# Performance work log

Hardware: AMD Instinct MI355X
Metric: run time of the kernel (lower is better)

Reference implementation:

```python
import jax, jax.numpy as jnp
import numpy as np
from jax import lax

GRID_SIZE = 3


def setup_inputs() -> dict:
    key = jax.random.key(0)
    k1, k2, k3 = jax.random.split(key, 3)
    B, Cin, Cout, H, W, KH, KW, G = 32, 64, 64, 64, 64, 3, 3, GRID_SIZE
    x = jax.random.normal(k1, (B, Cin, H, W), dtype=jnp.float32)
    scale_base = jax.random.normal(k2, (Cout, Cin, KH, KW), dtype=jnp.float32) * 0.1
    scale_spline = jnp.ones((Cout, Cin, KH, KW), dtype=jnp.float32)
    coeff = jax.random.normal(k3, (2, Cout, Cin, KH, KW, G), dtype=jnp.float32) * 0.02
    bias = jnp.zeros((Cout,), dtype=jnp.float32)
    return {"x": x, "scale_base": scale_base, "scale_spline": scale_spline, "coeff": coeff, "bias": bias}


def _conv(x, w, padding=1):
    return lax.conv_general_dilated(
        x, w, window_strides=(1, 1), padding=((padding, padding), (padding, padding)),
        dimension_numbers=("NCHW", "OIHW", "NCHW"))


def reference(x, scale_base, scale_spline, coeff, bias):
    B, Cin, H, W = x.shape
    Cout, _, KH, KW = scale_base.shape
    G = coeff.shape[-1]
    # Fourier feature expansion: cos(k*x), sin(k*x) for k = 1..G
    ks = jnp.arange(1, G + 1, dtype=x.dtype)
    xk = x[:, :, None] * ks[None, None, :, None, None]          # (B, Cin, G, H, W)
    feats = jnp.concatenate([jnp.cos(xk), jnp.sin(xk)], axis=2)  # (B, Cin, 2G, H, W)
    feats = feats.reshape(B, Cin * 2 * G, H, W)
    # Spline weights: coeff (2, Cout, Cin, KH, KW, G) scaled per-tap -> (Cout, Cin*2G, KH, KW)
    w = coeff * scale_spline[None, :, :, :, :, None]
    w = jnp.transpose(w, (1, 2, 0, 5, 3, 4)).reshape(Cout, Cin * 2 * G, KH, KW)
    # Base branch: SiLU(x) convolved with scale_base
    base = jax.nn.silu(x)
    out = _conv(base, scale_base) + _conv(feats, w)
    out = out + bias[None, :, None, None]
    return out
```

## Files before the change

### kernel.cpp

```cpp
#include <hip/hip_runtime.h>

typedef __attribute__((ext_vector_type(8))) short bf16x8;
typedef __attribute__((ext_vector_type(4))) float f32x4;

#define FROW   4224
#define FBUF   42240
#define BGRP   36864
#define LDS_TOT (2 * FBUF + 2 * BGRP)

static __device__ __forceinline__ unsigned short f2bf(float f) {
  union { float f; unsigned u; } v; v.f = f;
  unsigned r = v.u + 0x7fffu + ((v.u >> 16) & 1u);
  return (unsigned short)(r >> 16);
}

static __device__ __forceinline__ void gload16(const void* g, void* l) {
  __builtin_amdgcn_global_load_lds(
      (const __attribute__((address_space(1))) void*)g,
      (__attribute__((address_space(3))) void*)l, 16, 0, 0);
}

__global__ void pack_w_k(const float* __restrict__ sb, const float* __restrict__ ss,
                         const float* __restrict__ cf, unsigned short* __restrict__ wpk) {
  int idx = blockIdx.x * 256 + threadIdx.x;
  if (idx >= 126 * 64 * 32) return;
  int e = idx & 7;
  int q = (idx >> 3) & 3;
  int co = (idx >> 5) & 63;
  int rest = idx >> 11;
  int tap = rest % 9;
  int c2 = rest / 9;
  int c = c2 >> 1, half = c2 & 1;
  int ci = half * 32 + q * 8 + e;
  int kh = tap / 3, kw = tap % 3;
  int wi = ((co * 64 + ci) * 3 + kh) * 3 + kw;
  float v;
  if (c == 0) {
    v = sb[wi];
  } else {
    int s = (c - 1) / 3, g = (c - 1) % 3;
    v = cf[(s * 36864 + wi) * 3 + g] * ss[wi];
  }
  wpk[((c2 * 9 + tap) * 64 + co) * 32 + ((q ^ ((co >> 1) & 3)) << 3) + e] = f2bf(v);
}

__global__ void feats_k(const float* __restrict__ x, unsigned short* __restrict__ fg) {
  __shared__ __align__(16) unsigned short lds[64 * 456];
  const int b = blockIdx.x, h = blockIdx.y;
  const int tid = threadIdx.x;
  const int w = tid & 63, cig = tid >> 6;
  const int key = ((w + 1) >> 1) & 3;
  const int base = w * 456;
#pragma unroll
  for (int i = 0; i < 16; ++i) {
    int ci = cig * 16 + i;
    float v = x[(((size_t)b * 64 + ci) * 64 + h) * 64 + w];
    float sg = 1.0f / (1.0f + __expf(-v));
    float f0 = v * sg;
    float s1, c1;
    __sincosf(v, &s1, &c1);
    float c2v = c1 * c1 - s1 * s1, s2v = 2.0f * s1 * c1;
    float c3v = c1 * c2v - s1 * s2v, s3v = s1 * c2v + c1 * s2v;
    int q = ci >> 3;
    int half = q >> 2, qq = q & 3;
    int sl = (half * 4 + (qq ^ key)) * 8 + (ci & 7);
    lds[base + 0 * 64 + sl] = f2bf(f0);
    lds[base + 1 * 64 + sl] = f2bf(c1);
    lds[base + 2 * 64 + sl] = f2bf(c2v);
    lds[base + 3 * 64 + sl] = f2bf(c3v);
    lds[base + 4 * 64 + sl] = f2bf(s1);
    lds[base + 5 * 64 + sl] = f2bf(s2v);
    lds[base + 6 * 64 + sl] = f2bf(s3v);
  }
  __syncthreads();
#pragma unroll
  for (int k = 0; k < 14; ++k) {
    int u = tid + k * 256;
    int qs = u & 3;
    int ww = (u >> 2) & 63;
    int c2i = u >> 8;
    int cc = c2i >> 1, half = c2i & 1;
    uint4 v = *(const uint4*)&lds[ww * 456 + cc * 64 + (half * 4 + qs) * 8];
    unsigned short* dst = fg + ((size_t)(c2i * 32 + b) * 64 + h) * 2048 + (ww * 4 + qs) * 8;
    *(uint4*)dst = v;
  }
}

__global__ __launch_bounds__(512, 2) void gemm_k(
    const unsigned short* __restrict__ fg, const unsigned short* __restrict__ wpk,
    const float* __restrict__ bias, float* __restrict__ out) {
  extern __shared__ __align__(16) char smem[];
  const int b = blockIdx.x;
  const int h0 = blockIdx.y * 8;
  const int tid = threadIdx.x;
  const int lane = tid & 63;
  const int wid = tid >> 6;
  const int l15 = lane & 15;
  const int lg = lane >> 4;
  const int grp = wid >> 2;
  const int rowb = (wid & 3) * 2;
  const char* fgB = (const char*)fg;
  const char* wpkB = (const char*)wpk;

  for (int i = tid; i < 2 * FBUF / 4; i += 512) {
    int off = i * 4;
    int off2 = (off >= FBUF) ? off - FBUF : off;
    int row = off2 / FROW;
    int cb = off2 - row * FROW;
    int hh = h0 - 1 + row;
    bool staged = ((unsigned)hh < 64u) && (cb >= 64) && (cb < 4160);
    if (!staged) ((int*)smem)[i] = 0;
  }

  int aoff[4][3], boff[4];
#pragma unroll
  for (int cf = 0; cf < 4; ++cf) {
#pragma unroll
    for (int kw = 0; kw < 3; ++kw) {
      int col = cf * 16 + l15 + kw;
      aoff[cf][kw] = col * 64 + ((lg ^ ((col >> 1) & 3)) << 4);
    }
    int co = cf * 16 + l15;
    boff[cf] = co * 64 + ((lg ^ ((co >> 1) & 3)) << 4);
  }

#define STAGE_GRP(cn, fdst, bdst)                                                \
  for (int u = wid; u < 76; u += 8) {                                            \
    if (u < 40) {                                                                \
      int row = u >> 2, j = u & 3;                                               \
      int hh = h0 - 1 + row;                                                     \
      if ((unsigned)hh < 64u)                                                    \
        gload16(fgB + ((size_t)((cn) * 2048 + b * 64 + hh)) * 4096 +             \
                    j * 1024 + lane * 16,                                        \
                (fdst) + row * FROW + 64 + j * 1024);                            \
    } else {                                                                     \
      int t = u - 40;                                                            \
      int tap = t >> 2, part = t & 3;                                            \
      gload16(wpkB + (size_t)((cn) * 9 + tap) * 4096 + part * 1024 + lane * 16,  \
              (bdst) + tap * 4096 + part * 1024);                                \
    }                                                                            \
  }

  STAGE_GRP(0, smem, smem + 2 * FBUF);
  __syncthreads();

  f32x4 acc[2][4][4];
#pragma unroll
  for (int ro = 0; ro < 2; ++ro)
#pragma unroll
    for (int cfi = 0; cfi < 4; ++cfi)
#pragma unroll
      for (int nf = 0; nf < 4; ++nf)
#pragma unroll
        for (int qq = 0; qq < 4; ++qq) acc[ro][cfi][nf][qq] = 0.0f;

#define LOADT(T, Ar, Br)                                                         \
  {                                                                              \
    const int kh_ = (T) / 3, kw_ = (T) % 3;                                      \
    const char* r0 = f + (rowb + kh_) * FROW;                                    \
    const char* r1 = r0 + FROW;                                                  \
    _Pragma("unroll")                                                            \
    for (int cfi = 0; cfi < 4; ++cfi) {                                          \
      Ar[0][cfi] = *(const bf16x8*)(r0 + aoff[cfi][kw_]);                        \
      Ar[1][cfi] = *(const bf16x8*)(r1 + aoff[cfi][kw_]);                        \
    }                                                                            \
    _Pragma("unroll")                                                            \
    for (int nf = 0; nf < 4; ++nf)                                               \
      Br[nf] = *(const bf16x8*)(bgc + (T) * 4096 + boff[nf]);                    \
  }
#define MFMAT(Ar, Br)                                                            \
  {                                                                              \
    _Pragma("unroll")                                                            \
    for (int ro = 0; ro < 2; ++ro)                                               \
      _Pragma("unroll")                                                          \
      for (int cfi = 0; cfi < 4; ++cfi)                                          \
        _Pragma("unroll")                                                        \
        for (int nf = 0; nf < 4; ++nf)                                           \
          acc[ro][cfi][nf] = __builtin_amdgcn_mfma_f32_16x16x32_bf16(            \
              Ar[ro][cfi], Br[nf], acc[ro][cfi][nf], 0, 0, 0);                   \
  }

#define SGB(m, n) __builtin_amdgcn_sched_group_barrier((m), (n), 0);

  for (int c2 = 0; c2 < 14; ++c2) {
    const int cur = c2 & 1;
    const char* f = smem + (cur ? FBUF : 0);
    const char* bgc = smem + 2 * FBUF + (cur ? BGRP : 0);
    if (c2 < 13) {
      char* fnext = smem + (cur ? 0 : FBUF);
      char* bnext = smem + 2 * FBUF + (cur ? 0 : BGRP);
      STAGE_GRP(c2 + 1, fnext, bnext);
    }
    bf16x8 Aa[2][4], Ab[2][4], Ba[4], Bb[4];
    if (grp == 0) {
      LOADT(0, Aa, Ba)
      LOADT(1, Ab, Bb)
      MFMAT(Aa, Ba)
      LOADT(2, Aa, Ba)
      MFMAT(Ab, Bb)
      LOADT(3, Ab, Bb)
      MFMAT(Aa, Ba)
      LOADT(4, Aa, Ba)
      MFMAT(Ab, Bb)
      MFMAT(Aa, Ba)
      SGB(0x100, 12)
#pragma unroll
      for (int g = 0; g < 16; ++g) { SGB(0x8, 8) SGB(0x100, 3) }
#pragma unroll
      for (int g = 0; g < 4; ++g) { SGB(0x8, 8) }
    } else {
      LOADT(5, Aa, Ba)
      LOADT(6, Ab, Bb)
      MFMAT(Aa, Ba)
      LOADT(7, Aa, Ba)
      MFMAT(Ab, Bb)
      LOADT(8, Ab, Bb)
      MFMAT(Aa, Ba)
      MFMAT(Ab, Bb)
      SGB(0x100, 12)
#pragma unroll
      for (int g = 0; g < 12; ++g) { SGB(0x8, 8) SGB(0x100, 3) }
#pragma unroll
      for (int g = 0; g < 4; ++g) { SGB(0x8, 8) }
    }
    __syncthreads();
  }
#undef SGB
#undef LOADT
#undef MFMAT
#undef STAGE_GRP

  if (grp == 1) {
#pragma unroll
    for (int ro = 0; ro < 2; ++ro)
#pragma unroll
      for (int cfi = 0; cfi < 4; ++cfi)
#pragma unroll
        for (int nf = 0; nf < 4; ++nf) {
          int co = nf * 16 + l15;
          int pxl = (rowb + ro) * 64 + cfi * 16 + (lg << 2);
          float* p = (float*)smem + co * 512 + (pxl ^ ((co & 7) << 2));
          *(f32x4*)p = acc[ro][cfi][nf];
        }
  }
  __syncthreads();
  if (grp == 0) {
#pragma unroll
    for (int ro = 0; ro < 2; ++ro) {
      const int h = h0 + rowb + ro;
#pragma unroll
      for (int cfi = 0; cfi < 4; ++cfi) {
        int w4 = cfi * 16 + (lg << 2);
#pragma unroll
        for (int nf = 0; nf < 4; ++nf) {
          int co = nf * 16 + l15;
          int pxl = (rowb + ro) * 64 + cfi * 16 + (lg << 2);
          const float* p = (const float*)smem + co * 512 + (pxl ^ ((co & 7) << 2));
          f32x4 part = *(const f32x4*)p;
          float bv = bias[co];
          f32x4 v = acc[ro][cfi][nf];
          f32x4 res;
          res[0] = v[0] + part[0] + bv;
          res[1] = v[1] + part[1] + bv;
          res[2] = v[2] + part[2] + bv;
          res[3] = v[3] + part[3] + bv;
          *(f32x4*)(out + ((size_t)(b * 64 + co) * 64 + h) * 64 + w4) = res;
        }
      }
    }
  }
}

__global__ void naive_k(const float* __restrict__ x, const float* __restrict__ sb,
                        const float* __restrict__ ss, const float* __restrict__ cf,
                        const float* __restrict__ bias, float* __restrict__ out) {
  int idx = blockIdx.x * 256 + threadIdx.x;
  if (idx >= 32 * 64 * 64 * 64) return;
  int w = idx & 63, h = (idx >> 6) & 63, co = (idx >> 12) & 63, b = idx >> 18;
  float acc = bias[co];
  for (int ci = 0; ci < 64; ++ci) {
    for (int kh = 0; kh < 3; ++kh) {
      int hh = h + kh - 1;
      if ((unsigned)hh >= 64u) continue;
      for (int kw = 0; kw < 3; ++kw) {
        int ww = w + kw - 1;
        if ((unsigned)ww >= 64u) continue;
        float v = x[((b * 64 + ci) * 64 + hh) * 64 + ww];
        int wi = ((co * 64 + ci) * 3 + kh) * 3 + kw;
        float s1, c1; __sincosf(v, &s1, &c1);
        float c2 = c1 * c1 - s1 * s1, s2 = 2.f * s1 * c1;
        float c3 = c1 * c2 - s1 * s2, s3 = s1 * c2 + c1 * s2;
        float t = sb[wi] * (v / (1.f + __expf(-v)));
        t += ss[wi] * (cf[wi * 3] * c1 + cf[wi * 3 + 1] * c2 + cf[wi * 3 + 2] * c3 +
                       cf[(36864 + wi) * 3] * s1 + cf[(36864 + wi) * 3 + 1] * s2 +
                       cf[(36864 + wi) * 3 + 2] * s3);
        acc += t;
      }
    }
  }
  out[idx] = acc;
}

extern "C" void kernel_launch(void* const* d_in, const int* in_sizes, int n_in,
                              void* d_out, int out_size, void* d_ws, size_t ws_size,
                              hipStream_t stream) {
  const float* x = (const float*)d_in[0];
  const float* sb = (const float*)d_in[1];
  const float* ss = (const float*)d_in[2];
  const float* cf = (const float*)d_in[3];
  const float* bias = (const float*)d_in[4];
  float* out = (float*)d_out;

  const size_t FEATS_OFF = 1u << 20;
  const size_t NEED = FEATS_OFF + (size_t)14 * 32 * 64 * 4096;
  if (ws_size >= NEED) {
    unsigned short* wpk = (unsigned short*)d_ws;
    unsigned short* fg = (unsigned short*)((char*)d_ws + FEATS_OFF);
    pack_w_k<<<1008, 256, 0, stream>>>(sb, ss, cf, wpk);
    feats_k<<<dim3(32, 64), 256, 0, stream>>>(x, fg);
    (void)hipFuncSetAttribute((const void*)gemm_k,
                              hipFuncAttributeMaxDynamicSharedMemorySize, LDS_TOT);
    gemm_k<<<dim3(32, 8), 512, LDS_TOT, stream>>>(fg, wpk, bias, out);
  } else {
    naive_k<<<32768, 256, 0, stream>>>(x, sb, ss, cf, bias, out);
  }
}
```

Measured before the change: 96.73 us.

## Fuse Fourier/SiLU feature generation into GEMM kernel, dropping feats workspace

Removes the separate feats_k kernel, which wrote a large bf16 feature tensor to global memory. The GEMM kernel now reads x directly and computes SiLU, cos(kx) and sin(kx) per channel group into LDS while the previous group is being consumed, and still streams weights asynchronously. This removes a kernel launch and a large global write and read-back. In exchange the GEMM waves do transcendental math and synchronous global loads inside the pipeline, and each of the 14 groups recomputes from x, including the halo rows.

```diff
diff --git a/kernel.cpp b/kernel.cpp
--- a/kernel.cpp
+++ b/kernel.cpp
@@ -44,50 +44,8 @@
   wpk[((c2 * 9 + tap) * 64 + co) * 32 + ((q ^ ((co >> 1) & 3)) << 3) + e] = f2bf(v);
 }
 
-__global__ void feats_k(const float* __restrict__ x, unsigned short* __restrict__ fg) {
-  __shared__ __align__(16) unsigned short lds[64 * 456];
-  const int b = blockIdx.x, h = blockIdx.y;
-  const int tid = threadIdx.x;
-  const int w = tid & 63, cig = tid >> 6;
-  const int key = ((w + 1) >> 1) & 3;
-  const int base = w * 456;
-#pragma unroll
-  for (int i = 0; i < 16; ++i) {
-    int ci = cig * 16 + i;
-    float v = x[(((size_t)b * 64 + ci) * 64 + h) * 64 + w];
-    float sg = 1.0f / (1.0f + __expf(-v));
-    float f0 = v * sg;
-    float s1, c1;
-    __sincosf(v, &s1, &c1);
-    float c2v = c1 * c1 - s1 * s1, s2v = 2.0f * s1 * c1;
-    float c3v = c1 * c2v - s1 * s2v, s3v = s1 * c2v + c1 * s2v;
-    int q = ci >> 3;
-    int half = q >> 2, qq = q & 3;
-    int sl = (half * 4 + (qq ^ key)) * 8 + (ci & 7);
-    lds[base + 0 * 64 + sl] = f2bf(f0);
-    lds[base + 1 * 64 + sl] = f2bf(c1);
-    lds[base + 2 * 64 + sl] = f2bf(c2v);
-    lds[base + 3 * 64 + sl] = f2bf(c3v);
-    lds[base + 4 * 64 + sl] = f2bf(s1);
-    lds[base + 5 * 64 + sl] = f2bf(s2v);
-    lds[base + 6 * 64 + sl] = f2bf(s3v);
-  }
-  __syncthreads();
-#pragma unroll
-  for (int k = 0; k < 14; ++k) {
-    int u = tid + k * 256;
-    int qs = u & 3;
-    int ww = (u >> 2) & 63;
-    int c2i = u >> 8;
-    int cc = c2i >> 1, half = c2i & 1;
-    uint4 v = *(const uint4*)&lds[ww * 456 + cc * 64 + (half * 4 + qs) * 8];
-    unsigned short* dst = fg + ((size_t)(c2i * 32 + b) * 64 + h) * 2048 + (ww * 4 + qs) * 8;
-    *(uint4*)dst = v;
-  }
-}
-
 __global__ __launch_bounds__(512, 2) void gemm_k(
-    const unsigned short* __restrict__ fg, const unsigned short* __restrict__ wpk,
+    const float* __restrict__ x, const unsigned short* __restrict__ wpk,
     const float* __restrict__ bias, float* __restrict__ out) {
   extern __shared__ __align__(16) char smem[];
   const int b = blockIdx.x;
@@ -99,8 +57,13 @@
   const int lg = lane >> 4;
   const int grp = wid >> 2;
   const int rowb = (wid & 3) * 2;
-  const char* fgB = (const char*)fg;
   const char* wpkB = (const char*)wpk;
+
+  const int fw = tid & 63;
+  const int fkq = (wid + (fw >> 3)) & 7;
+  const int fcol = fw + 1;
+  const int fslot = ((fkq >> 1) ^ ((fcol >> 1) & 3));
+  const int foff = fcol * 64 + fslot * 16 + (fkq & 1) * 8;
 
   for (int i = tid; i < 2 * FBUF / 4; i += 512) {
     int off = i * 4;
@@ -124,24 +87,47 @@
     boff[cf] = co * 64 + ((lg ^ ((co >> 1) & 3)) << 4);
   }
 
-#define STAGE_GRP(cn, fdst, bdst)                                                \
-  for (int u = wid; u < 76; u += 8) {                                            \
-    if (u < 40) {                                                                \
-      int row = u >> 2, j = u & 3;                                               \
-      int hh = h0 - 1 + row;                                                     \
-      if ((unsigned)hh < 64u)                                                    \
-        gload16(fgB + ((size_t)((cn) * 2048 + b * 64 + hh)) * 4096 +             \
-                    j * 1024 + lane * 16,                                        \
-                (fdst) + row * FROW + 64 + j * 1024);                            \
-    } else {                                                                     \
-      int t = u - 40;                                                            \
-      int tap = t >> 2, part = t & 3;                                            \
-      gload16(wpkB + (size_t)((cn) * 9 + tap) * 4096 + part * 1024 + lane * 16,  \
-              (bdst) + tap * 4096 + part * 1024);                                \
+#define STAGE_B(cn, bdst)                                                        \
+  for (int u = wid; u < 36; u += 8) {                                            \
+    gload16(wpkB + (size_t)((cn) * 9 + (u >> 2)) * 4096 + (u & 3) * 1024 +       \
+                lane * 16,                                                       \
+            (bdst) + (u >> 2) * 4096 + (u & 3) * 1024);                          \
+  }
+
+#define FEATGEN(cn, fdst)                                                        \
+  {                                                                              \
+    const int c_ = (cn) >> 1, half_ = (cn) & 1;                                  \
+    const float kf_ = (float)(c_ <= 3 ? c_ : c_ - 3);                            \
+    const float* xb_ = x + (((size_t)b * 64 + half_ * 32 + 4 * fkq) * 64) * 64 + fw; \
+    float xv[10][4];                                                             \
+    _Pragma("unroll")                                                            \
+    for (int r = 0; r < 10; ++r) {                                               \
+      int hh = h0 - 1 + r;                                                       \
+      if ((unsigned)hh < 64u) {                                                  \
+        _Pragma("unroll")                                                        \
+        for (int j = 0; j < 4; ++j) xv[r][j] = xb_[((size_t)j * 64 + hh) * 64];  \
+      }                                                                          \
     }                                                                            \
-  }
-
-  STAGE_GRP(0, smem, smem + 2 * FBUF);
+    _Pragma("unroll")                                                            \
+    for (int r = 0; r < 10; ++r) {                                               \
+      int hh = h0 - 1 + r;                                                       \
+      if ((unsigned)hh < 64u) {                                                  \
+        unsigned long long pk = 0;                                               \
+        _Pragma("unroll")                                                        \
+        for (int j = 0; j < 4; ++j) {                                            \
+          float v = xv[r][j], val;                                               \
+          if (c_ == 0)      val = v / (1.0f + __expf(-v));                       \
+          else if (c_ <= 3) val = __cosf(kf_ * v);                               \
+          else              val = __sinf(kf_ * v);                               \
+          pk |= (unsigned long long)f2bf(val) << (16 * j);                       \
+        }                                                                        \
+        *(unsigned long long*)((fdst) + r * FROW + foff) = pk;                   \
+      }                                                                          \
+    }                                                                            \
+  }
+
+  FEATGEN(0, smem)
+  STAGE_B(0, smem + 2 * FBUF)
   __syncthreads();
 
   f32x4 acc[2][4][4];
@@ -179,7 +165,6 @@
           acc[ro][cfi][nf] = __builtin_amdgcn_mfma_f32_16x16x32_bf16(            \
               Ar[ro][cfi], Br[nf], acc[ro][cfi][nf], 0, 0, 0);                   \
   }
-
 #define SGB(m, n) __builtin_amdgcn_sched_group_barrier((m), (n), 0);
 
   for (int c2 = 0; c2 < 14; ++c2) {
@@ -189,7 +174,8 @@
     if (c2 < 13) {
       char* fnext = smem + (cur ? 0 : FBUF);
       char* bnext = smem + 2 * FBUF + (cur ? 0 : BGRP);
-      STAGE_GRP(c2 + 1, fnext, bnext);
+      STAGE_B(c2 + 1, bnext)
+      FEATGEN(c2 + 1, fnext)
     }
     bf16x8 Aa[2][4], Ab[2][4], Ba[4], Bb[4];
     if (grp == 0) {
@@ -228,7 +214,8 @@
 #undef SGB
 #undef LOADT
 #undef MFMAT
-#undef STAGE_GRP
+#undef STAGE_B
+#undef FEATGEN
 
   if (grp == 1) {
 #pragma unroll
@@ -311,16 +298,13 @@
   const float* bias = (const float*)d_in[4];
   float* out = (float*)d_out;
 
-  const size_t FEATS_OFF = 1u << 20;
-  const size_t NEED = FEATS_OFF + (size_t)14 * 32 * 64 * 4096;
+  const size_t NEED = 1u << 20;
   if (ws_size >= NEED) {
     unsigned short* wpk = (unsigned short*)d_ws;
-    unsigned short* fg = (unsigned short*)((char*)d_ws + FEATS_OFF);
     pack_w_k<<<1008, 256, 0, stream>>>(sb, ss, cf, wpk);
-    feats_k<<<dim3(32, 64), 256, 0, stream>>>(x, fg);
     (void)hipFuncSetAttribute((const void*)gemm_k,
                               hipFuncAttributeMaxDynamicSharedMemorySize, LDS_TOT);
-    gemm_k<<<dim3(32, 8), 512, LDS_TOT, stream>>>(fg, wpk, bias, out);
+    gemm_k<<<dim3(32, 8), 512, LDS_TOT, stream>>>(x, wpk, bias, out);
   } else {
     naive_k<<<32768, 256, 0, stream>>>(x, sb, ss, cf, bias, out);
   }
```

Result: slower. 136.8 us (+41.4%).
